# Kernel tuning notes

Hardware: AMD Instinct MI355X
Metric: run time of the kernel (lower is better)

Reference implementation:

```python
import jax, jax.numpy as jnp
import numpy as np

NUM_NODE = 65536      # destination nodes in this layer
NUM_SRC = 262144      # rows of x (sampled source nodes)
DEG = 16              # uniform degree -> num_edge = NUM_NODE*DEG
NUM_EDGE = NUM_NODE * DEG
IN_CH = 128
HID_CH = 128
NUM_REL = 8


def setup_inputs() -> dict:
    key = jax.random.key(0)
    ks = jax.random.split(key, 8)
    x = jax.random.normal(ks[0], (NUM_SRC, IN_CH), dtype=jnp.float32)
    # glorot-style init for relation weights [R, in, hid]
    scale = jnp.sqrt(6.0 / (IN_CH + HID_CH))
    weight = jax.random.uniform(ks[1], (NUM_REL, IN_CH, HID_CH), dtype=jnp.float32,
                                minval=-scale, maxval=scale)
    history_buffer = jax.random.normal(ks[2], (NUM_NODE, HID_CH), dtype=jnp.float32)
    ptr = jnp.arange(NUM_NODE + 1, dtype=jnp.int64) * DEG  # uniform-degree CSR
    idx = jax.random.randint(ks[3], (NUM_EDGE,), 0, NUM_SRC, dtype=jnp.int64)
    edge_types = jax.random.randint(ks[4], (NUM_EDGE,), 0, NUM_REL, dtype=jnp.int64)
    used_mask = jax.random.uniform(ks[5], (NUM_SRC,)) < 0.95
    # history_map: -1 means no cached entry; >=0 means overwrite from buffer
    history_map = jax.random.randint(ks[6], (NUM_NODE,), -1, 5, dtype=jnp.int64)
    return {
        "x": x, "weight": weight, "history_buffer": history_buffer,
        "ptr": ptr, "idx": idx, "edge_types": edge_types,
        "used_mask": used_mask, "history_map": history_map,
        "history_size": HID_CH, "num_node": NUM_NODE,
    }


def reference(x, weight, history_buffer, ptr, idx, edge_types, used_mask,
              history_map, history_size, num_node):
    num_rel = weight.shape[0]
    num_edge = idx.shape[0]          # == ptr[num_node] by construction
    hid = weight.shape[2]
    fdt = x.dtype

    deg = ptr[1:num_node + 1] - ptr[:num_node]                 # [N]
    dst = jnp.repeat(jnp.arange(num_node), deg,
                     total_repeat_length=num_edge)             # [E]
    src = idx                                                  # [E]
    # edges whose source is not "used" get relation num_rel -> no weight group
    rel = jnp.where(used_mask[src], edge_types, num_rel)       # [E]

    # relation-grouped GEMM + gather, expressed as masked accumulation
    # (avoids materializing [E, in, hid] gathered weights)
    msg = jnp.zeros((num_edge, hid), dtype=fdt)
    for r in range(num_rel):
        h_r = x @ weight[r]                                    # [Nsrc, hid]
        msg = msg + jnp.where((rel == r)[:, None], h_r[src], jnp.zeros((), fdt))

    out = jax.ops.segment_sum(msg, dst, num_segments=num_node) # scatter-add
    out = out / deg.astype(fdt)[:, None]                       # degree norm

    if history_size > 0:
        cached = (history_map != -1)[:, None]
        out = jnp.where(cached, history_buffer, out)           # history overwrite
    # original returns (out, his) with his aliasing out
    return out
```

## Files before the change

### kernel.cpp

```cpp
#include <hip/hip_runtime.h>
#include <hip/hip_bf16.h>
#include <stdint.h>

typedef __attribute__((ext_vector_type(4))) float f32x4;
typedef __attribute__((ext_vector_type(8))) short bf16x8;

#define NCH  128
#define NREL 8
#define NSEG 32
#define SEGCAP 2048

__device__ __forceinline__ unsigned short f2bf(float f) {
    unsigned u = __builtin_bit_cast(unsigned, f);
    u += 0x7fffu + ((u >> 16) & 1u);
    return (unsigned short)(u >> 16);
}

__device__ __forceinline__ bool mask_used(const unsigned char* um, int stride, int s) {
    if (stride == 1) return um[s] != 0;
    if (stride == 4) return ((const int*)um)[s] != 0;
    return ((const long long*)um)[s] != 0;
}

__global__ __launch_bounds__(256)
void k_prep(const float* __restrict__ W, unsigned short* __restrict__ Wb,
            int* __restrict__ cn, const unsigned char* __restrict__ um_raw) {
    int o = blockIdx.x * 256 + threadIdx.x;
    if (o < NREL * NCH * NCH) {
        int kk = o & 31;
        int h  = (o >> 5) & (NCH - 1);
        int kt = o >> 12;
        Wb[o] = f2bf(W[(kt * 32 + kk) * NCH + h]);
    }
    if (blockIdx.x == 0) {
        __shared__ unsigned sA, sB;
        const int t = threadIdx.x;
        if (t == 0) { sA = 0; sB = 0; }
        if (t < NSEG) cn[16 + t * 16] = 0;
        __syncthreads();
        unsigned a = 0, b = 0;
        #pragma unroll 4
        for (int p = t; p < 1024; p += 256) {
            unsigned v = um_raw[p];
            if ((p & 3) != 0) a |= v;
            if ((p & 7) == 4) b |= v;
        }
        if (a) atomicOr(&sA, 1u);
        if (b) atomicOr(&sB, 1u);
        __syncthreads();
        if (t == 0) cn[1] = sA ? 1 : (sB ? 4 : 8);
    }
}

__global__ __launch_bounds__(256)
void k_hist(const float* __restrict__ hb, const int* __restrict__ hm,
            const int* __restrict__ hs, float* __restrict__ out,
            int* __restrict__ cn, int* __restrict__ glist, int num_node) {
    __shared__ int ncList[32];
    __shared__ int cList[32];
    __shared__ int nNC, nC, gbase;
    const int t = threadIdx.x;
    if (t == 0) { nNC = 0; nC = 0; }
    __syncthreads();
    const int n = blockIdx.x * 32 + t;
    if (t < 32 && n < num_node) {
        const bool cached = (hs[0] > 0) && (hm[n] != -1);
        if (cached) { int p = atomicAdd(&nC, 1);  cList[p]  = n; }
        else        { int p = atomicAdd(&nNC, 1); ncList[p] = n; }
    }
    __syncthreads();
    const int hw = t >> 5, l = t & 31;
    int   node[4];
    f32x4 v[4];
    #pragma unroll 4
    for (int j = 0; j < 4; ++j) {
        const int i = hw + j * 8;
        node[j] = (i < nC) ? cList[i] : -1;
        if (node[j] >= 0)
            v[j] = *(const f32x4*)(hb + (long)node[j] * NCH + l * 4);
    }
    #pragma unroll 4
    for (int j = 0; j < 4; ++j) {
        if (node[j] >= 0)
            *(f32x4*)(out + (long)node[j] * NCH + l * 4) = v[j];
    }
    const int seg = blockIdx.x & (NSEG - 1);
    if (t == 0) gbase = atomicAdd(&cn[16 + seg * 16], nNC);
    __syncthreads();
    if (t < nNC) glist[seg * SEGCAP + gbase + t] = ncList[t];
}

__global__ __launch_bounds__(512, 2)
void k_main(const float* __restrict__ x, const unsigned short* __restrict__ Wb,
            const int* __restrict__ ptr, const int* __restrict__ idx,
            const int* __restrict__ et, const unsigned char* __restrict__ um,
            const int* __restrict__ cn, const int* __restrict__ glist,
            float* __restrict__ out) {
    __shared__ __align__(16) char As[16 * NREL * NCH * 2];
    __shared__ int   nid[16];
    __shared__ float invdeg[16];

    const int seg   = blockIdx.x & (NSEG - 1);
    const int grp   = blockIdx.x >> 5;
    const int cntS  = cn[16 + seg * 16];
    const int base  = grp * 16;
    if (base >= cntS) return;
    const int mstride = cn[1];
    const int t = threadIdx.x;
    if (t < 16) {
        const int i = base + t;
        nid[t]    = (i < cntS) ? glist[seg * SEGCAP + i] : -1;
        invdeg[t] = 0.0f;
    }
    __syncthreads();

    const int hw    = t >> 5;
    const int l     = t & 31;
    const int lbase = t & 32;
    const int n     = nid[hw];

    if (n >= 0) {
        const int p0 = ptr[n], p1 = ptr[n + 1];
        const int deg = p1 - p0;
        if (l == 0) invdeg[hw] = (deg > 0) ? 1.0f / (float)deg : 0.0f;
        int myPk = NREL << 24;
        if (l < 16 && (p0 + l) < p1) {
            const int e  = p0 + l;
            const int s  = idx[e];
            const int tt = et[e];
            myPk = s | (((mask_used(um, mstride, s) && tt >= 0 && tt < NREL)
                         ? tt : NREL) << 24);
        }
        int   pk[16];
        f32x4 xv[16];
        #pragma unroll 16
        for (int e = 0; e < 16; ++e) {
            pk[e] = __shfl(myPk, lbase + e, 64);
            xv[e] = *(const f32x4*)(x + (long)(pk[e] & 0xFFFFFF) * NCH + l * 4);
        }
        float acc[NREL][4];
        #pragma unroll
        for (int q = 0; q < NREL; ++q)
            #pragma unroll
            for (int j = 0; j < 4; ++j) acc[q][j] = 0.0f;
        #pragma unroll 16
        for (int e = 0; e < 16; ++e) {
            const int r = pk[e] >> 24;
            #pragma unroll
            for (int q = 0; q < NREL; ++q) {
                const float sel = (r == q) ? 1.0f : 0.0f;
                acc[q][0] += sel * xv[e].x;
                acc[q][1] += sel * xv[e].y;
                acc[q][2] += sel * xv[e].z;
                acc[q][3] += sel * xv[e].w;
            }
        }
        for (int e = p0 + 16; e < p1; ++e) {
            const int s  = idx[e];
            const int tt = et[e];
            if (mask_used(um, mstride, s) && tt >= 0 && tt < NREL) {
                const f32x4 w = *(const f32x4*)(x + (long)s * NCH + l * 4);
                #pragma unroll
                for (int q = 0; q < NREL; ++q) {
                    const float sel = (tt == q) ? 1.0f : 0.0f;
                    acc[q][0] += sel * w.x;
                    acc[q][1] += sel * w.y;
                    acc[q][2] += sel * w.z;
                    acc[q][3] += sel * w.w;
                }
            }
        }
        #pragma unroll
        for (int q = 0; q < NREL; ++q) {
            ushort4 pkv;
            pkv.x = f2bf(acc[q][0]); pkv.y = f2bf(acc[q][1]);
            pkv.z = f2bf(acc[q][2]); pkv.w = f2bf(acc[q][3]);
            const int eb   = (q * NCH + l * 4) * 2;
            const int addr = (hw * 2048 + eb) ^ ((hw & 7) << 4);
            *(ushort4*)(As + addr) = pkv;
        }
    }
    __syncthreads();

    const int wv   = t >> 6;
    const int lane = t & 63;
    const int row  = lane & 15;
    const int koff = (lane >> 4) * 8;
    const int col0 = wv * 16 + row;
    f32x4 c0 = {0.f, 0.f, 0.f, 0.f};
    #pragma unroll 8
    for (int kt = 0; kt < 32; ++kt) {
        const int aaddr = (row * 2048 + (kt * 32 + koff) * 2) ^ ((row & 7) << 4);
        const bf16x8 a  = *(const bf16x8*)(As + aaddr);
        const bf16x8 b0 = *(const bf16x8*)(Wb + ((kt * NCH + col0) << 5) + koff);
        c0 = __builtin_amdgcn_mfma_f32_16x16x32_bf16(a, b0, c0, 0, 0, 0);
    }

    __syncthreads();
    float* Cs = (float*)As;
    {
        const int r4 = (lane >> 4) * 4;
        #pragma unroll
        for (int j = 0; j < 4; ++j) {
            const int rr = r4 + j;
            Cs[rr * NCH + col0] = c0[j] * invdeg[rr];
        }
    }
    __syncthreads();
    {
        const int nn = nid[hw];
        if (nn >= 0) {
            const f32x4 vv = *(const f32x4*)(Cs + hw * NCH + l * 4);
            *(f32x4*)(out + (long)nn * NCH + l * 4) = vv;
        }
    }
}

extern "C" void kernel_launch(void* const* d_in, const int* in_sizes, int n_in,
                              void* d_out, int out_size, void* d_ws, size_t ws_size,
                              hipStream_t stream) {
    const float*         x   = (const float*)d_in[0];
    const float*         W   = (const float*)d_in[1];
    const float*         hb  = (const float*)d_in[2];
    const int*           ptr = (const int*)d_in[3];
    const int*           idx = (const int*)d_in[4];
    const int*           et  = (const int*)d_in[5];
    const unsigned char* um  = (const unsigned char*)d_in[6];
    const int*           hm  = (const int*)d_in[7];
    const int*           hs  = (const int*)d_in[8];
    float* out = (float*)d_out;

    const int num_node = in_sizes[7];

    size_t off = 2560;
    int* cn    = (int*)d_ws;
    int* glist = (int*)((char*)d_ws + off);       off += (size_t)NSEG * SEGCAP * 4;
    unsigned short* Wb = (unsigned short*)((char*)d_ws + off);

    k_prep<<<(NREL * NCH * NCH + 255) / 256, 256, 0, stream>>>(W, Wb, cn, um);
    k_hist<<<(num_node + 31) / 32, 256, 0, stream>>>(hb, hm, hs, out, cn, glist, num_node);
    k_main<<<(num_node + 15) / 16, 512, 0, stream>>>(x, Wb, ptr, idx, et, um, cn, glist, out);
}
```

Measured before the change: 50.82 us.

## Use ballot compaction in history pass, nontemporal stores, raise k_main occupancy

The history classification kernel replaces shared-memory atomics and one barrier with wave-level ballot plus popcount compaction. Output stores in both k_hist and k_main become nontemporal, so they bypass cache retention. k_main's launch bounds change from 2 to 4 blocks per CU. That forces fewer registers per thread and may cause spills in the 16-edge gather loop, which keeps many f32x4 values live.

Result: no change. 50.93 us (+0.2%).

```diff
diff --git a/kernel.cpp b/kernel.cpp
--- a/kernel.cpp
+++ b/kernel.cpp
@@ -56,41 +56,46 @@
 void k_hist(const float* __restrict__ hb, const int* __restrict__ hm,
             const int* __restrict__ hs, float* __restrict__ out,
             int* __restrict__ cn, int* __restrict__ glist, int num_node) {
-    __shared__ int ncList[32];
-    __shared__ int cList[32];
-    __shared__ int nNC, nC, gbase;
+    __shared__ int cList[32], ncList[32];
+    __shared__ int nCs, nNCs, gbase;
     const int t = threadIdx.x;
-    if (t == 0) { nNC = 0; nC = 0; }
-    __syncthreads();
-    const int n = blockIdx.x * 32 + t;
-    if (t < 32 && n < num_node) {
-        const bool cached = (hs[0] > 0) && (hm[n] != -1);
-        if (cached) { int p = atomicAdd(&nC, 1);  cList[p]  = n; }
-        else        { int p = atomicAdd(&nNC, 1); ncList[p] = n; }
-    }
-    __syncthreads();
+    if (t < 64) {
+        const int n = blockIdx.x * 32 + t;
+        const bool valid  = (t < 32) && (n < num_node);
+        const bool cached = valid && (hs[0] > 0) && (hm[n] != -1);
+        const bool nc     = valid && !cached;
+        const unsigned long long mC  = __ballot(cached);
+        const unsigned long long mNC = __ballot(nc);
+        const unsigned long long below = (1ull << t) - 1;
+        if (cached) cList[__popcll(mC & below)]   = n;
+        if (nc)     ncList[__popcll(mNC & below)] = n;
+        if (t == 0) { nCs = __popcll(mC); nNCs = __popcll(mNC); }
+    }
+    __syncthreads();
+    const int myC = nCs, myNC = nNCs;
     const int hw = t >> 5, l = t & 31;
     int   node[4];
     f32x4 v[4];
     #pragma unroll 4
     for (int j = 0; j < 4; ++j) {
         const int i = hw + j * 8;
-        node[j] = (i < nC) ? cList[i] : -1;
+        node[j] = (i < myC) ? cList[i] : -1;
         if (node[j] >= 0)
             v[j] = *(const f32x4*)(hb + (long)node[j] * NCH + l * 4);
     }
     #pragma unroll 4
     for (int j = 0; j < 4; ++j) {
         if (node[j] >= 0)
-            *(f32x4*)(out + (long)node[j] * NCH + l * 4) = v[j];
+            __builtin_nontemporal_store(v[j],
+                (f32x4*)(out + (long)node[j] * NCH + l * 4));
     }
     const int seg = blockIdx.x & (NSEG - 1);
-    if (t == 0) gbase = atomicAdd(&cn[16 + seg * 16], nNC);
-    __syncthreads();
-    if (t < nNC) glist[seg * SEGCAP + gbase + t] = ncList[t];
-}
-
-__global__ __launch_bounds__(512, 2)
+    if (t == 0) gbase = atomicAdd(&cn[16 + seg * 16], myNC);
+    __syncthreads();
+    if (t < myNC) glist[seg * SEGCAP + gbase + t] = ncList[t];
+}
+
+__global__ __launch_bounds__(512, 4)
 void k_main(const float* __restrict__ x, const unsigned short* __restrict__ Wb,
             const int* __restrict__ ptr, const int* __restrict__ idx,
             const int* __restrict__ et, const unsigned char* __restrict__ um,
@@ -211,7 +216,8 @@
         const int nn = nid[hw];
         if (nn >= 0) {
             const f32x4 vv = *(const f32x4*)(Cs + hw * NCH + l * 4);
-            *(f32x4*)(out + (long)nn * NCH + l * 4) = vv;
+            __builtin_nontemporal_store(vv,
+                (f32x4*)(out + (long)nn * NCH + l * 4));
         }
     }
 }
```
